# Kernel tuning notes

Measured on AMD Instinct MI355X. Metric: run time of the kernel, lower is better.

## Reference

```python
import jax, jax.numpy as jnp
import numpy as np

N_HEADS = 4
D_HEAD = 64
SCALE = D_HEAD ** -0.5


def setup_inputs() -> dict:
    key = jax.random.key(0)
    k0, k1, k2, k3, k4 = jax.random.split(key, 5)
    C = 256
    return {
        "x": jax.random.normal(k0, (32, C, 32, 32), dtype=jnp.float32),
        "W_qkv": jax.random.normal(k1, (C, 3 * N_HEADS * D_HEAD), dtype=jnp.float32) * 0.02,
        "b_qkv": jax.random.normal(k2, (3 * N_HEADS * D_HEAD,), dtype=jnp.float32) * 0.02,
        "W_out": jax.random.normal(k3, (C, C), dtype=jnp.float32) * 0.02,
        "b_out": jax.random.normal(k4, (C,), dtype=jnp.float32) * 0.02,
    }


def reference(x, W_qkv, b_qkv, W_out, b_out):
    b, c, h, w = x.shape
    # [B, C, H, W] -> [B, S, C], S = H*W  (NOTE: GroupNorm is defined in the
    # original module but never applied in forward; we match that exactly.)
    xs = x.reshape(b, c, h * w).transpose(0, 2, 1)
    qkv = (xs @ W_qkv + b_qkv).reshape(b, -1, N_HEADS, 3 * D_HEAD)
    q, k, v = jnp.split(qkv, 3, axis=-1)  # each [B, S, H, D]
    scores = jnp.einsum('bihd,bjhd->bijh', q, k) * SCALE  # [B, S, S, H]
    attn = jax.nn.softmax(scores, axis=2)  # softmax over key index j
    res = jnp.einsum('bijh,bjhd->bihd', attn, v).reshape(b, -1, N_HEADS * D_HEAD)
    res = res @ W_out + b_out + xs
    return res.transpose(0, 2, 1).reshape(b, c, h, w)
```

## Files before the change

kernel.cpp:

```cpp
#include <hip/hip_runtime.h>

#define NH 4
#define DH 64
#define SS 1024
#define CC 256
#define BB 32

typedef __attribute__((ext_vector_type(8))) short short8;
typedef __attribute__((ext_vector_type(4))) float floatx4;

#define MFMA16(a, b, c) __builtin_amdgcn_mfma_f32_16x16x32_bf16(a, b, c, 0, 0, 0)

#define QSCALE 0.18033688011112042f

__device__ __forceinline__ short f2bf(float f) {
    union { float f; unsigned u; } v; v.f = f;
    unsigned r = (v.u + 0x7fffu + ((v.u >> 16) & 1u)) >> 16;
    return (short)r;
}
__device__ __forceinline__ short f2bf_trunc(float f) {
    union { float f; unsigned u; } v; v.f = f;
    return (short)(v.u >> 16);
}

__global__ __launch_bounds__(256) void k_transpose_x(const float* __restrict__ x,
                                                     short* __restrict__ xs) {
    __shared__ float tile[64][65];
    int b = blockIdx.z;
    int s0 = blockIdx.x * 64;
    int c0 = blockIdx.y * 64;
    int t = threadIdx.x;
    int tx = t & 63, ty = t >> 6;
    for (int i = 0; i < 16; ++i) {
        int c = ty + i * 4;
        tile[tx][c] = x[((b * CC) + (c0 + c)) * SS + s0 + tx];
    }
    __syncthreads();
    for (int i = 0; i < 8; ++i) {
        int s = (t >> 5) + i * 8;
        int cp = (t & 31) * 2;
        short2 v;
        v.x = f2bf(tile[s][cp]);
        v.y = f2bf(tile[s][cp + 1]);
        *(short2*)(&xs[((b * SS) + (s0 + s)) * CC + c0 + cp]) = v;
    }
}

__global__ __launch_bounds__(256) void k_transpose_w(const float* __restrict__ Wqkv,
                                                     const float* __restrict__ Wout,
                                                     short* __restrict__ Wqkv_t,
                                                     short* __restrict__ Wout_t) {
    int idx = blockIdx.x * 256 + threadIdx.x;
    if (idx < 768 * 256) {
        int n = idx >> 8, k = idx & 255;
        Wqkv_t[idx] = f2bf(Wqkv[k * 768 + n]);
    } else {
        int j = idx - 768 * 256;
        int c = j >> 8, k = j & 255;
        Wout_t[j] = f2bf(Wout[k * 256 + c]);
    }
}

__global__ __launch_bounds__(256) void k_qkv(const short* __restrict__ xs,
                                             const short* __restrict__ Wt,
                                             const float* __restrict__ bqkv,
                                             short* __restrict__ qw,
                                             short* __restrict__ kw,
                                             short* __restrict__ vtw) {
    __shared__ short smem[10240];
    short* As = smem;
    short* Bs = smem + 5120;
    int m0 = blockIdx.x * 128;
    int n0 = blockIdx.y * 128;
    int t = threadIdx.x;
    int lane = t & 63, wid = t >> 6;
    int wr = wid >> 1, wc = wid & 1;
    int c16 = lane & 15, qd = lane >> 4;

    floatx4 acc[4][4] = {};
    short8 pa[2], pb[2];

    {
        for (int j = 0; j < 2; ++j) {
            int id = j * 256 + t, row = id >> 2, cc = id & 3;
            pa[j] = *(const short8*)(&xs[(m0 + row) * CC + cc * 8]);
            pb[j] = *(const short8*)(&Wt[(n0 + row) * CC + cc * 8]);
        }
    }
    for (int kt = 0; kt < 8; ++kt) {
        if (kt) __syncthreads();
        for (int j = 0; j < 2; ++j) {
            int id = j * 256 + t, row = id >> 2, cc = id & 3;
            *(short8*)(&As[row * 40 + cc * 8]) = pa[j];
            *(short8*)(&Bs[row * 40 + cc * 8]) = pb[j];
        }
        __syncthreads();
        if (kt < 7) {
            for (int j = 0; j < 2; ++j) {
                int id = j * 256 + t, row = id >> 2, cc = id & 3;
                pa[j] = *(const short8*)(&xs[(m0 + row) * CC + (kt + 1) * 32 + cc * 8]);
                pb[j] = *(const short8*)(&Wt[(n0 + row) * CC + (kt + 1) * 32 + cc * 8]);
            }
        }
        short8 av[4], bv[4];
        for (int i = 0; i < 4; ++i) {
            av[i] = *(const short8*)(&As[(wr * 64 + i * 16 + c16) * 40 + qd * 8]);
            bv[i] = *(const short8*)(&Bs[(wc * 64 + i * 16 + c16) * 40 + qd * 8]);
        }
        for (int mi = 0; mi < 4; ++mi)
            for (int ni = 0; ni < 4; ++ni)
                acc[mi][ni] = MFMA16(av[mi], bv[ni], acc[mi][ni]);
    }

    int b = m0 >> 10, sbase = m0 & 1023;
    float bias4[4];
    for (int ni = 0; ni < 4; ++ni)
        bias4[ni] = bqkv[n0 + wc * 64 + ni * 16 + c16];

    for (int half = 0; half < 2; ++half) {
        int seg = (n0 >> 6) + half;
        int sel = seg % 3, h = seg / 3;
        int bh = b * NH + h;
        __syncthreads();
        if (wc == half) {
            if (sel == 2) {
                for (int mi = 0; mi < 4; ++mi)
                    for (int ni = 0; ni < 4; ++ni)
                        for (int r = 0; r < 4; ++r)
                            smem[(ni * 16 + c16) * 136 + wr * 64 + mi * 16 + qd * 4 + r] =
                                f2bf(acc[mi][ni][r] + bias4[ni]);
            } else {
                float sc = (sel == 0) ? QSCALE : 1.f;
                for (int mi = 0; mi < 4; ++mi)
                    for (int ni = 0; ni < 4; ++ni)
                        for (int r = 0; r < 4; ++r)
                            smem[(wr * 64 + mi * 16 + qd * 4 + r) * 80 + ni * 16 + c16] =
                                f2bf((acc[mi][ni][r] + bias4[ni]) * sc);
            }
        }
        __syncthreads();
        if (sel == 2) {
            for (int i = 0; i < 4; ++i) {
                int d = (t >> 4) + i * 16;
                int sc8 = (t & 15) * 8;
                *(short8*)(&vtw[(bh * DH + d) * SS + sbase + sc8]) =
                    *(const short8*)(&smem[d * 136 + sc8]);
            }
        } else {
            short* dst = (sel == 0) ? qw : kw;
            for (int i = 0; i < 4; ++i) {
                int srow = (t >> 3) + i * 32;
                int d8 = (t & 7) * 8;
                *(short8*)(&dst[(bh * SS + sbase + srow) * DH + d8]) =
                    *(const short8*)(&smem[srow * 80 + d8]);
            }
        }
    }
}

__global__ __launch_bounds__(256) void k_attn(const short* __restrict__ qw,
                                              const short* __restrict__ kw,
                                              const short* __restrict__ vtw,
                                              short* __restrict__ res) {
    __shared__ short Ks[64 * 72];
    __shared__ short Vts[64 * 72];
    __shared__ short Ps[4 * 16 * 72];
    int bid = blockIdx.x;
    int q0 = (bid >> 7) * 128;
    int bh = bid & 127;
    int t = threadIdx.x;
    int lane = t & 63, w = t >> 6;
    int c16 = lane & 15, qd = lane >> 4;
    const short* qp = qw + bh * SS * DH;
    const short* kp = kw + bh * SS * DH;
    const short* vp = vtw + bh * DH * SS;

    short8 qfrag[2][2];
    for (int g = 0; g < 2; ++g)
        for (int ks = 0; ks < 2; ++ks)
            qfrag[g][ks] = *(const short8*)(
                &qp[(q0 + g * 64 + w * 16 + c16) * DH + ks * 32 + qd * 8]);

    float l_i[2][4] = {};
    floatx4 o_acc[2][4] = {};

    short8 kreg[2], vreg[2];
    for (int j = 0; j < 2; ++j) {
        int id = j * 256 + t, row = id >> 3, cc = id & 7;
        kreg[j] = *(const short8*)(&kp[row * DH + cc * 8]);
        vreg[j] = *(const short8*)(&vp[row * SS + cc * 8]);
    }

    int pb = w * 16 * 72;
    for (int kt = 0; kt < 16; ++kt) {
        if (kt) __syncthreads();
        for (int j = 0; j < 2; ++j) {
            int id = j * 256 + t, row = id >> 3, cc = id & 7;
            *(short8*)(&Ks[row * 72 + cc * 8]) = kreg[j];
            *(short8*)(&Vts[row * 72 + cc * 8]) = vreg[j];
        }
        __syncthreads();
        if (kt < 15) {
            for (int j = 0; j < 2; ++j) {
                int id = j * 256 + t, row = id >> 3, cc = id & 7;
                kreg[j] = *(const short8*)(&kp[((kt + 1) * 64 + row) * DH + cc * 8]);
                vreg[j] = *(const short8*)(&vp[row * SS + (kt + 1) * 64 + cc * 8]);
            }
        }

        short8 kf[2][4], vf[2][4];
        for (int ks = 0; ks < 2; ++ks)
            for (int ni = 0; ni < 4; ++ni) {
                kf[ks][ni] = *(const short8*)(&Ks[(ni * 16 + c16) * 72 + ks * 32 + qd * 8]);
                vf[ks][ni] = *(const short8*)(&Vts[(ni * 16 + c16) * 72 + ks * 32 + qd * 8]);
            }

        for (int g = 0; g < 2; ++g) {
            floatx4 sacc[4] = {};
            for (int ks = 0; ks < 2; ++ks)
                for (int ni = 0; ni < 4; ++ni)
                    sacc[ni] = MFMA16(qfrag[g][ks], kf[ks][ni], sacc[ni]);

            for (int ni = 0; ni < 4; ++ni)
                for (int rr = 0; rr < 4; ++rr) {
                    float e = __builtin_amdgcn_exp2f(sacc[ni][rr]);
                    l_i[g][rr] += e;
                    Ps[pb + (qd * 4 + rr) * 72 + ni * 16 + c16] = f2bf_trunc(e);
                }

            for (int ks = 0; ks < 2; ++ks) {
                short8 pa = *(const short8*)(&Ps[pb + c16 * 72 + ks * 32 + qd * 8]);
                for (int di = 0; di < 4; ++di)
                    o_acc[g][di] = MFMA16(pa, vf[ks][di], o_acc[g][di]);
            }
        }
    }

    for (int g = 0; g < 2; ++g)
        for (int rr = 0; rr < 4; ++rr) {
            float l = l_i[g][rr];
            for (int off = 1; off < 16; off <<= 1) l += __shfl_xor(l, off);
            l_i[g][rr] = 1.f / l;
        }

    int b = bh >> 2, h = bh & 3;
    for (int g = 0; g < 2; ++g)
        for (int di = 0; di < 4; ++di)
            for (int rr = 0; rr < 4; ++rr) {
                int s = q0 + g * 64 + w * 16 + qd * 4 + rr;
                res[(b * SS + s) * CC + h * DH + di * 16 + c16] =
                    f2bf(o_acc[g][di][rr] * l_i[g][rr]);
            }
}

__global__ __launch_bounds__(256) void k_out(const short* __restrict__ res,
                                             const short* __restrict__ Wot,
                                             const float* __restrict__ bout,
                                             const float* __restrict__ x,
                                             float* __restrict__ out) {
    __shared__ short As[128 * 40];
    __shared__ short Bs[128 * 40];
    int b = blockIdx.z;
    int m0 = blockIdx.y * 128;
    int n0 = blockIdx.x * 128;
    int t = threadIdx.x;
    int lane = t & 63, wid = t >> 6;
    int wr = wid >> 1, wc = wid & 1;
    int c16 = lane & 15, qd = lane >> 4;

    floatx4 acc[4][4] = {};
    short8 pa[2], pbv[2];
    for (int j = 0; j < 2; ++j) {
        int id = j * 256 + t, row = id >> 2, cc = id & 3;
        pa[j] = *(const short8*)(&Wot[(m0 + row) * CC + cc * 8]);
        pbv[j] = *(const short8*)(&res[(b * SS + n0 + row) * CC + cc * 8]);
    }

    for (int kt = 0; kt < 8; ++kt) {
        if (kt) __syncthreads();
        for (int j = 0; j < 2; ++j) {
            int id = j * 256 + t, row = id >> 2, cc = id & 3;
            *(short8*)(&As[row * 40 + cc * 8]) = pa[j];
            *(short8*)(&Bs[row * 40 + cc * 8]) = pbv[j];
        }
        __syncthreads();
        if (kt < 7) {
            for (int j = 0; j < 2; ++j) {
                int id = j * 256 + t, row = id >> 2, cc = id & 3;
                pa[j] = *(const short8*)(&Wot[(m0 + row) * CC + (kt + 1) * 32 + cc * 8]);
                pbv[j] = *(const short8*)(&res[(b * SS + n0 + row) * CC + (kt + 1) * 32 + cc * 8]);
            }
        }
        short8 av[4], bv[4];
        for (int i = 0; i < 4; ++i) {
            av[i] = *(const short8*)(&As[(wr * 64 + i * 16 + c16) * 40 + qd * 8]);
            bv[i] = *(const short8*)(&Bs[(wc * 64 + i * 16 + c16) * 40 + qd * 8]);
        }
        for (int mi = 0; mi < 4; ++mi)
            for (int ni = 0; ni < 4; ++ni)
                acc[mi][ni] = MFMA16(av[mi], bv[ni], acc[mi][ni]);
    }

    for (int mi = 0; mi < 4; ++mi) {
        for (int r = 0; r < 4; ++r) {
            int c = m0 + wr * 64 + mi * 16 + qd * 4 + r;
            float bias = bout[c];
            for (int ni = 0; ni < 4; ++ni) {
                int s = n0 + wc * 64 + ni * 16 + c16;
                float v = acc[mi][ni][r] + bias + x[((b * CC) + c) * SS + s];
                out[((b * CC) + c) * SS + s] = v;
            }
        }
    }
}

extern "C" void kernel_launch(void* const* d_in, const int* in_sizes, int n_in,
                              void* d_out, int out_size, void* d_ws, size_t ws_size,
                              hipStream_t stream) {
    const float* x    = (const float*)d_in[0];
    const float* Wqkv = (const float*)d_in[1];
    const float* bqkv = (const float*)d_in[2];
    const float* Wout = (const float*)d_in[3];
    const float* bout = (const float*)d_in[4];
    float* out = (float*)d_out;

    char* ws = (char*)d_ws;
    short* xs_res = (short*)(ws);
    short* qw     = (short*)(ws + 16777216);
    short* kw     = (short*)(ws + 33554432);
    short* vtw    = (short*)(ws + 50331648);
    short* Wqkv_t = (short*)(ws + 67108864);
    short* Wout_t = (short*)(ws + 67502080);

    k_transpose_x<<<dim3(16, 4, 32), 256, 0, stream>>>(x, xs_res);
    k_transpose_w<<<dim3(1024), 256, 0, stream>>>(Wqkv, Wout, Wqkv_t, Wout_t);
    k_qkv<<<dim3(256, 6), 256, 0, stream>>>(xs_res, Wqkv_t, bqkv, qw, kw, vtw);
    k_attn<<<dim3(1024), 256, 0, stream>>>(qw, kw, vtw, xs_res);
    k_out<<<dim3(8, 2, 32), 256, 0, stream>>>(xs_res, Wout_t, bout, x, out);
}
```

Before: 190.3 us.

## Transpose attention MFMA operands for packed P stores and merge prep kernels

The attention kernel swaps MFMA operand order so S and O are computed transposed. Each lane then holds four consecutive keys or output columns for a single query row. That lets P be written to LDS as packed 64-bit stores, shrinks the row-sum reduction to two shuffles, and lets the output be written as packed uint2 stores instead of scalar shorts. Separately, the x-transpose and weight-transpose kernels are merged into one launch to save a kernel launch. The padded P buffer stride changes to 76, which may alter bank-conflict behaviour.

```diff
diff --git a/kernel.cpp b/kernel.cpp
--- a/kernel.cpp
+++ b/kernel.cpp
@@ -18,46 +18,55 @@
     unsigned r = (v.u + 0x7fffu + ((v.u >> 16) & 1u)) >> 16;
     return (short)r;
 }
-__device__ __forceinline__ short f2bf_trunc(float f) {
+__device__ __forceinline__ unsigned bfrn(float f) {
     union { float f; unsigned u; } v; v.f = f;
-    return (short)(v.u >> 16);
-}
-
-__global__ __launch_bounds__(256) void k_transpose_x(const float* __restrict__ x,
-                                                     short* __restrict__ xs) {
-    __shared__ float tile[64][65];
-    int b = blockIdx.z;
-    int s0 = blockIdx.x * 64;
-    int c0 = blockIdx.y * 64;
-    int t = threadIdx.x;
-    int tx = t & 63, ty = t >> 6;
-    for (int i = 0; i < 16; ++i) {
-        int c = ty + i * 4;
-        tile[tx][c] = x[((b * CC) + (c0 + c)) * SS + s0 + tx];
-    }
-    __syncthreads();
-    for (int i = 0; i < 8; ++i) {
-        int s = (t >> 5) + i * 8;
-        int cp = (t & 31) * 2;
-        short2 v;
-        v.x = f2bf(tile[s][cp]);
-        v.y = f2bf(tile[s][cp + 1]);
-        *(short2*)(&xs[((b * SS) + (s0 + s)) * CC + c0 + cp]) = v;
-    }
-}
-
-__global__ __launch_bounds__(256) void k_transpose_w(const float* __restrict__ Wqkv,
-                                                     const float* __restrict__ Wout,
-                                                     short* __restrict__ Wqkv_t,
-                                                     short* __restrict__ Wout_t) {
-    int idx = blockIdx.x * 256 + threadIdx.x;
-    if (idx < 768 * 256) {
-        int n = idx >> 8, k = idx & 255;
-        Wqkv_t[idx] = f2bf(Wqkv[k * 768 + n]);
+    return (v.u + 0x7fffu + ((v.u >> 16) & 1u)) >> 16;
+}
+__device__ __forceinline__ unsigned pk2_trunc(float a, float b) {
+    union { float f; unsigned u; } ua, ub; ua.f = a; ub.f = b;
+    return (ua.u >> 16) | (ub.u & 0xFFFF0000u);
+}
+__device__ __forceinline__ unsigned pk2_rn(float a, float b) {
+    return bfrn(a) | (bfrn(b) << 16);
+}
+
+__global__ __launch_bounds__(256) void k_prep(const float* __restrict__ x,
+                                              const float* __restrict__ Wqkv,
+                                              const float* __restrict__ Wout,
+                                              short* __restrict__ xs,
+                                              short* __restrict__ Wqkv_t,
+                                              short* __restrict__ Wout_t) {
+    int bid = blockIdx.x;
+    if (bid < 2048) {
+        __shared__ float tile[64][65];
+        int b = bid >> 6;
+        int s0 = ((bid >> 2) & 15) * 64;
+        int c0 = (bid & 3) * 64;
+        int t = threadIdx.x;
+        int tx = t & 63, ty = t >> 6;
+        for (int i = 0; i < 16; ++i) {
+            int c = ty + i * 4;
+            tile[tx][c] = x[((b * CC) + (c0 + c)) * SS + s0 + tx];
+        }
+        __syncthreads();
+        for (int i = 0; i < 8; ++i) {
+            int s = (t >> 5) + i * 8;
+            int cp = (t & 31) * 2;
+            short2 v;
+            v.x = f2bf(tile[s][cp]);
+            v.y = f2bf(tile[s][cp + 1]);
+            *(short2*)(&xs[((b * SS) + (s0 + s)) * CC + c0 + cp]) = v;
+        }
     } else {
-        int j = idx - 768 * 256;
-        int c = j >> 8, k = j & 255;
-        Wout_t[j] = f2bf(Wout[k * 256 + c]);
+        int idx = (bid - 2048) * 256 + threadIdx.x;
+        if (idx < 768 * 256) {
+            int n = idx >> 8, k = idx & 255;
+            Wqkv_t[idx] = f2bf(Wqkv[k * 768 + n]);
+        } else {
+            int j = idx - 768 * 256;
+            int c = j >> 8, k = j & 255;
+            Wout_t[j] = f2bf(Wout[k * 256 + c]);
+        }
     }
 }
 
@@ -162,9 +171,9 @@
                                               const short* __restrict__ kw,
                                               const short* __restrict__ vtw,
                                               short* __restrict__ res) {
-    __shared__ short Ks[64 * 72];
-    __shared__ short Vts[64 * 72];
-    __shared__ short Ps[4 * 16 * 72];
+    __shared__ __align__(16) short Ks[64 * 72];
+    __shared__ __align__(16) short Vts[64 * 72];
+    __shared__ __align__(16) short Pt[4 * 16 * 76];
     int bid = blockIdx.x;
     int q0 = (bid >> 7) * 128;
     int bh = bid & 127;
@@ -181,7 +190,7 @@
             qfrag[g][ks] = *(const short8*)(
                 &qp[(q0 + g * 64 + w * 16 + c16) * DH + ks * 32 + qd * 8]);
 
-    float l_i[2][4] = {};
+    float l_i[2] = {};
     floatx4 o_acc[2][4] = {};
 
     short8 kreg[2], vreg[2];
@@ -191,7 +200,7 @@
         vreg[j] = *(const short8*)(&vp[row * SS + cc * 8]);
     }
 
-    int pb = w * 16 * 72;
+    int pbase = w * 16 * 76;
     for (int kt = 0; kt < 16; ++kt) {
         if (kt) __syncthreads();
         for (int j = 0; j < 2; ++j) {
@@ -210,47 +219,56 @@
 
         short8 kf[2][4], vf[2][4];
         for (int ks = 0; ks < 2; ++ks)
-            for (int ni = 0; ni < 4; ++ni) {
-                kf[ks][ni] = *(const short8*)(&Ks[(ni * 16 + c16) * 72 + ks * 32 + qd * 8]);
-                vf[ks][ni] = *(const short8*)(&Vts[(ni * 16 + c16) * 72 + ks * 32 + qd * 8]);
+            for (int ji = 0; ji < 4; ++ji) {
+                kf[ks][ji] = *(const short8*)(&Ks[(ji * 16 + c16) * 72 + ks * 32 + qd * 8]);
+                vf[ks][ji] = *(const short8*)(&Vts[(ji * 16 + c16) * 72 + ks * 32 + qd * 8]);
             }
 
         for (int g = 0; g < 2; ++g) {
             floatx4 sacc[4] = {};
             for (int ks = 0; ks < 2; ++ks)
-                for (int ni = 0; ni < 4; ++ni)
-                    sacc[ni] = MFMA16(qfrag[g][ks], kf[ks][ni], sacc[ni]);
-
-            for (int ni = 0; ni < 4; ++ni)
-                for (int rr = 0; rr < 4; ++rr) {
-                    float e = __builtin_amdgcn_exp2f(sacc[ni][rr]);
-                    l_i[g][rr] += e;
-                    Ps[pb + (qd * 4 + rr) * 72 + ni * 16 + c16] = f2bf_trunc(e);
-                }
-
-            for (int ks = 0; ks < 2; ++ks) {
-                short8 pa = *(const short8*)(&Ps[pb + c16 * 72 + ks * 32 + qd * 8]);
+                for (int ji = 0; ji < 4; ++ji)
+                    sacc[ji] = MFMA16(kf[ks][ji], qfrag[g][ks], sacc[ji]);
+
+            for (int ji = 0; ji < 4; ++ji) {
+                float e0 = __builtin_amdgcn_exp2f(sacc[ji][0]);
+                float e1 = __builtin_amdgcn_exp2f(sacc[ji][1]);
+                float e2 = __builtin_amdgcn_exp2f(sacc[ji][2]);
+                float e3 = __builtin_amdgcn_exp2f(sacc[ji][3]);
+                l_i[g] += (e0 + e1) + (e2 + e3);
+                uint2 pw;
+                pw.x = pk2_trunc(e0, e1);
+                pw.y = pk2_trunc(e2, e3);
+                *(uint2*)(&Pt[pbase + c16 * 76 + ji * 16 + qd * 4]) = pw;
+            }
+
+            for (int ks2 = 0; ks2 < 2; ++ks2) {
+                short8 pf = *(const short8*)(&Pt[pbase + c16 * 76 + ks2 * 32 + qd * 8]);
                 for (int di = 0; di < 4; ++di)
-                    o_acc[g][di] = MFMA16(pa, vf[ks][di], o_acc[g][di]);
-            }
-        }
-    }
-
-    for (int g = 0; g < 2; ++g)
-        for (int rr = 0; rr < 4; ++rr) {
-            float l = l_i[g][rr];
-            for (int off = 1; off < 16; off <<= 1) l += __shfl_xor(l, off);
-            l_i[g][rr] = 1.f / l;
-        }
+                    o_acc[g][di] = MFMA16(vf[ks2][di], pf, o_acc[g][di]);
+            }
+        }
+    }
+
+    for (int g = 0; g < 2; ++g) {
+        float l = l_i[g];
+        l += __shfl_xor(l, 16);
+        l += __shfl_xor(l, 32);
+        l_i[g] = 1.f / l;
+    }
 
     int b = bh >> 2, h = bh & 3;
-    for (int g = 0; g < 2; ++g)
-        for (int di = 0; di < 4; ++di)
-            for (int rr = 0; rr < 4; ++rr) {
-                int s = q0 + g * 64 + w * 16 + qd * 4 + rr;
-                res[(b * SS + s) * CC + h * DH + di * 16 + c16] =
-                    f2bf(o_acc[g][di][rr] * l_i[g][rr]);
-            }
+    for (int g = 0; g < 2; ++g) {
+        int s = q0 + g * 64 + w * 16 + c16;
+        long base = (long)(b * SS + s) * CC + h * DH;
+        float inv = l_i[g];
+        for (int di = 0; di < 4; ++di) {
+            uint2 ow;
+            ow.x = pk2_rn(o_acc[g][di][0] * inv, o_acc[g][di][1] * inv);
+            ow.y = pk2_rn(o_acc[g][di][2] * inv, o_acc[g][di][3] * inv);
+            *(uint2*)(&res[base + di * 16 + qd * 4]) = ow;
+        }
+    }
 }
 
 __global__ __launch_bounds__(256) void k_out(const short* __restrict__ res,
@@ -332,8 +350,7 @@
     short* Wqkv_t = (short*)(ws + 67108864);
     short* Wout_t = (short*)(ws + 67502080);
 
-    k_transpose_x<<<dim3(16, 4, 32), 256, 0, stream>>>(x, xs_res);
-    k_transpose_w<<<dim3(1024), 256, 0, stream>>>(Wqkv, Wout, Wqkv_t, Wout_t);
+    k_prep<<<dim3(3072), 256, 0, stream>>>(x, Wqkv, Wout, xs_res, Wqkv_t, Wout_t);
     k_qkv<<<dim3(256, 6), 256, 0, stream>>>(xs_res, Wqkv_t, bqkv, qw, kw, vtw);
     k_attn<<<dim3(1024), 256, 0, stream>>>(qw, kw, vtw, xs_res);
     k_out<<<dim3(8, 2, 32), 256, 0, stream>>>(xs_res, Wout_t, bout, x, out);
```

Result: faster. 184.4 us (-3.1%).
